# Kernel tuning notes

Measured on AMD Instinct MI355X. Metric: run time of the kernel, lower is better.

The kernel has to match this reference:

```python
import jax, jax.numpy as jnp
import numpy as np

N_NODES = 50000
N_EDGES = 800000
IN_DIM = 128
EMB = 64
EDGE_DIM = 6
N_LAYERS = 4
OUT_DIM = 1


def setup_inputs() -> dict:
    key = jax.random.key(0)
    ks = jax.random.split(key, 20)
    s = 0.05
    inp = {
        "x": jax.random.normal(ks[0], (N_NODES, IN_DIM), jnp.float32),
        "edge_index": jax.random.randint(ks[1], (2, N_EDGES), 0, N_NODES, jnp.int64),
        "edge_attr": jax.random.normal(ks[2], (N_EDGES, EDGE_DIM), jnp.float32),
        # input projection
        "lin_in_w": jax.random.normal(ks[3], (IN_DIM, EMB), jnp.float32) * s,
        "lin_in_b": jnp.zeros((EMB,), jnp.float32),
        # stacked per-layer MLP params: message MLP psi: (2*EMB+EDGE_DIM)->EMB->EMB
        "msg_w1": jax.random.normal(ks[4], (N_LAYERS, 2 * EMB + EDGE_DIM, EMB), jnp.float32) * s,
        "msg_b1": jnp.zeros((N_LAYERS, EMB), jnp.float32),
        "msg_w2": jax.random.normal(ks[5], (N_LAYERS, EMB, EMB), jnp.float32) * s,
        "msg_b2": jnp.zeros((N_LAYERS, EMB), jnp.float32),
        # update MLP phi: (2*EMB)->EMB->EMB
        "upd_w1": jax.random.normal(ks[6], (N_LAYERS, 2 * EMB, EMB), jnp.float32) * s,
        "upd_b1": jnp.zeros((N_LAYERS, EMB), jnp.float32),
        "upd_w2": jax.random.normal(ks[7], (N_LAYERS, EMB, EMB), jnp.float32) * s,
        "upd_b2": jnp.zeros((N_LAYERS, EMB), jnp.float32),
        # output head
        "pred_w": jax.random.normal(ks[8], (EMB, OUT_DIM), jnp.float32) * s,
        "pred_b": jnp.zeros((OUT_DIM,), jnp.float32),
    }
    return inp


def reference(x, edge_index, edge_attr, lin_in_w, lin_in_b,
              msg_w1, msg_b1, msg_w2, msg_b2,
              upd_w1, upd_b1, upd_w2, upd_b2,
              pred_w, pred_b):
    n = x.shape[0]
    src = edge_index[0]  # h_j: source nodes
    dst = edge_index[1]  # h_i: target nodes (aggregation index in PyG default flow)
    h = x @ lin_in_w + lin_in_b  # (n, EMB)
    n_layers = msg_w1.shape[0]
    for l in range(n_layers):
        # message: psi([h_i, h_j, e_ij])  -> (E, EMB)
        m = jnp.concatenate([h[dst], h[src], edge_attr], axis=-1)
        m = jax.nn.relu(m @ msg_w1[l] + msg_b1[l])
        m = jax.nn.relu(m @ msg_w2[l] + msg_b2[l])
        # aggregate: scatter-add over target nodes
        agg = jax.ops.segment_sum(m, dst, num_segments=n)
        # update: phi([h, m_i]) with residual connection (h = h + conv(h))
        u = jnp.concatenate([h, agg], axis=-1)
        u = jax.nn.relu(u @ upd_w1[l] + upd_b1[l])
        u = jax.nn.relu(u @ upd_w2[l] + upd_b2[l])
        h = h + u
    out = h @ pred_w + pred_b  # (n, OUT_DIM)
    return jnp.sum(out, axis=-2)  # (OUT_DIM,)
```

## Files before the change

kernel.cpp:

```cpp
#include <hip/hip_runtime.h>


typedef __attribute__((ext_vector_type(8))) short short8;
typedef __attribute__((ext_vector_type(4))) float float4v;

__device__ __forceinline__ unsigned short f2bf(float f) {
    unsigned int u = __float_as_uint(f);
    unsigned int r = u + 0x7fff + ((u >> 16) & 1);
    return (unsigned short)(r >> 16);
}
__device__ __forceinline__ float bf2f(unsigned short u) {
    return __uint_as_float(((unsigned int)u) << 16);
}

#define MFMA16(a, b, c) __builtin_amdgcn_mfma_f32_16x16x32_bf16(a, b, c, 0, 0, 0)

struct bfpair { short hi, lo; };
__device__ __forceinline__ bfpair wsplit(float wv) {
    bfpair p;
    unsigned short h = f2bf(wv);
    float hf = __uint_as_float(((unsigned int)h) << 16);
    p.hi = (short)h;
    p.lo = (short)f2bf(wv - hf);
    return p;
}

#define WP_TOTAL 106496
#define OFF_IN   0
#define OFF_PRE(l)  (8192  + (l) * 8192)
#define OFF_MW2(l)  (40960 + (l) * 4096)
#define OFF_UW1(l)  (57344 + (l) * 8192)
#define OFF_UW2(l)  (90112 + (l) * 4096)

__global__ __launch_bounds__(256) void k_wprep(const float* __restrict__ lin_w,
        const float* __restrict__ mw1, const float* __restrict__ mw2,
        const float* __restrict__ uw1, const float* __restrict__ uw2,
        unsigned short* __restrict__ H, unsigned short* __restrict__ L) {
    const int tid = blockIdx.x * 256 + threadIdx.x;
    if (tid >= WP_TOTAL) return;
    float val;
    if (tid < 8192) {
        int rem = tid;
        int nt = rem >> 11, kf = (rem >> 9) & 3;
        int lane = (rem >> 3) & 63, j = rem & 7;
        int k = kf * 32 + (lane >> 4) * 8 + j;
        val = lin_w[k * 64 + nt * 16 + (lane & 15)];
    } else if (tid < 40960) {
        int t = tid - 8192, layer = t >> 13, rem = t & 8191;
        int nt = rem >> 10, kf = (rem >> 9) & 1;
        int lane = (rem >> 3) & 63, j = rem & 7;
        int k = kf * 32 + (lane >> 4) * 8 + j;
        const float* w1 = mw1 + (size_t)layer * 134 * 64;
        val = (nt < 4) ? w1[k * 64 + nt * 16 + (lane & 15)]
                       : w1[(64 + k) * 64 + (nt - 4) * 16 + (lane & 15)];
    } else if (tid < 57344) {
        int t = tid - 40960, layer = t >> 12, rem = t & 4095;
        int nt = rem >> 10, kf = (rem >> 9) & 1;
        int lane = (rem >> 3) & 63, j = rem & 7;
        int k = kf * 32 + (lane >> 4) * 8 + j;
        val = mw2[(size_t)layer * 4096 + k * 64 + nt * 16 + (lane & 15)];
    } else if (tid < 90112) {
        int t = tid - 57344, layer = t >> 13, rem = t & 8191;
        int nt = rem >> 11, kf = (rem >> 9) & 3;
        int lane = (rem >> 3) & 63, j = rem & 7;
        int k = kf * 32 + (lane >> 4) * 8 + j;
        val = uw1[(size_t)layer * 8192 + k * 64 + nt * 16 + (lane & 15)];
    } else {
        int t = tid - 90112, layer = t >> 12, rem = t & 4095;
        int nt = rem >> 10, kf = (rem >> 9) & 1;
        int lane = (rem >> 3) & 63, j = rem & 7;
        int k = kf * 32 + (lane >> 4) * 8 + j;
        val = uw2[(size_t)layer * 4096 + k * 64 + nt * 16 + (lane & 15)];
    }
    bfpair p = wsplit(val);
    H[tid] = (unsigned short)p.hi;
    L[tid] = (unsigned short)p.lo;
}

#define LOADFRAG(dst, arr, nt, KF, kf) \
    dst = *(const short8*)&arr[((((nt) * (KF)) + (kf)) * 64 + lane) * 8]

__global__ __launch_bounds__(256) void k_hist(const int* __restrict__ dst,
        int* __restrict__ deg, int nEdges) {
    int e = blockIdx.x * blockDim.x + threadIdx.x;
    if (e < nEdges) atomicAdd(&deg[dst[e]], 1);
}

__global__ __launch_bounds__(256) void k_scan1(const int* __restrict__ deg,
        int* __restrict__ local, int* __restrict__ bsum, int nNodes) {
    __shared__ int sm[256];
    const int t = threadIdx.x;
    const int n = blockIdx.x * 256 + t;
    int v = (n < nNodes) ? deg[n] : 0;
    sm[t] = v;
    __syncthreads();
    for (int off = 1; off < 256; off <<= 1) {
        int u = (t >= off) ? sm[t - off] : 0;
        __syncthreads();
        sm[t] += u;
        __syncthreads();
    }
    if (n < nNodes) local[n] = sm[t] - v;
    if (t == 255) bsum[blockIdx.x] = sm[255];
}

__global__ __launch_bounds__(256) void k_scan2(int* __restrict__ bsum, int nB) {
    __shared__ int sm[256];
    const int t = threadIdx.x;
    int v = (t < nB) ? bsum[t] : 0;
    sm[t] = v;
    __syncthreads();
    for (int off = 1; off < 256; off <<= 1) {
        int u = (t >= off) ? sm[t - off] : 0;
        __syncthreads();
        sm[t] += u;
        __syncthreads();
    }
    if (t < nB) bsum[t] = sm[t] - v;
}

__global__ __launch_bounds__(256) void k_scan3(const int* __restrict__ local,
        const int* __restrict__ bsum, int* __restrict__ cursor, int nNodes) {
    int n = blockIdx.x * 256 + threadIdx.x;
    if (n < nNodes) cursor[n] = bsum[blockIdx.x] + local[n];
}

__global__ __launch_bounds__(256) void k_scatter(const int* __restrict__ src,
        const int* __restrict__ dst, const float* __restrict__ ea,
        int* __restrict__ cursor, int* __restrict__ col_src,
        int* __restrict__ dst_s, float* __restrict__ ea_s, int nEdges) {
    int e = blockIdx.x * blockDim.x + threadIdx.x;
    if (e < nEdges) {
        int d = dst[e];
        int pos = atomicAdd(&cursor[d], 1);
        col_src[pos] = src[e];
        dst_s[pos] = d;
        const float* p = ea + (size_t)e * 6;
        float* q = ea_s + (size_t)pos * 6;
#pragma unroll
        for (int j = 0; j < 6; ++j) q[j] = p[j];
    }
}


__global__ __launch_bounds__(256) void k_in(const float* __restrict__ x,
        const unsigned short* __restrict__ wh, const unsigned short* __restrict__ wl,
        const float* __restrict__ bia, float* __restrict__ h, int nNodes) {
    const int lane = threadIdx.x & 63;
    const int wib  = threadIdx.x >> 6;
    const int quad = lane >> 4, col = lane & 15;
    __shared__ unsigned short sm[4][16 * 136];
    unsigned short* __restrict__ mt = sm[wib];

    short8 bh[4][4], bl[4][4];
#pragma unroll
    for (int nt = 0; nt < 4; ++nt)
#pragma unroll
        for (int kf = 0; kf < 4; ++kf) {
            LOADFRAG(bh[nt][kf], wh, nt, 4, kf);
            LOADFRAG(bl[nt][kf], wl, nt, 4, kf);
        }
    float bv[4];
#pragma unroll
    for (int nt = 0; nt < 4; ++nt) bv[nt] = bia[nt * 16 + col];

    const int nTiles = (nNodes + 15) >> 4;
    const int wid = blockIdx.x * 4 + wib;
    const int nw  = gridDim.x * 4;
    for (int tile = wid; tile < nTiles; tile += nw) {
        const int base = tile * 16;
#pragma unroll
        for (int j = 0; j < 16; ++j) {
            int row = min(base + j, nNodes - 1);
            mt[j * 136 + lane]      = f2bf(x[(size_t)row * 128 + lane]);
            mt[j * 136 + 64 + lane] = f2bf(x[(size_t)row * 128 + 64 + lane]);
        }
        __builtin_amdgcn_s_waitcnt(0);
        short8 a[4];
#pragma unroll
        for (int kf = 0; kf < 4; ++kf)
            a[kf] = *(const short8*)&mt[col * 136 + kf * 32 + quad * 8];
#pragma unroll
        for (int nt = 0; nt < 4; ++nt) {
            float4v c = {0.f, 0.f, 0.f, 0.f};
#pragma unroll
            for (int kf = 0; kf < 4; ++kf) c = MFMA16(a[kf], bh[nt][kf], c);
#pragma unroll
            for (int kf = 0; kf < 4; ++kf) c = MFMA16(a[kf], bl[nt][kf], c);
#pragma unroll
            for (int r = 0; r < 4; ++r) {
                int row = base + quad * 4 + r;
                if (row < nNodes)
                    h[(size_t)row * 64 + nt * 16 + col] = c[r] + bv[nt];
            }
        }
    }
}

__global__ __launch_bounds__(256) void k_pre(const float* __restrict__ h,
        const unsigned short* __restrict__ wh, const unsigned short* __restrict__ wl,
        const float* __restrict__ b1m,
        unsigned short* __restrict__ P, unsigned short* __restrict__ Q,
        int nNodes) {
    const int lane = threadIdx.x & 63;
    const int wib  = threadIdx.x >> 6;
    const int quad = lane >> 4, col = lane & 15;
    __shared__ unsigned short sm[4][16 * 72];
    unsigned short* __restrict__ mt = sm[wib];

    short8 bh[8][2], bl[8][2];
#pragma unroll
    for (int nt = 0; nt < 8; ++nt)
#pragma unroll
        for (int kf = 0; kf < 2; ++kf) {
            LOADFRAG(bh[nt][kf], wh, nt, 2, kf);
            LOADFRAG(bl[nt][kf], wl, nt, 2, kf);
        }
    float bv1[4];
#pragma unroll
    for (int nt = 0; nt < 4; ++nt) bv1[nt] = b1m[nt * 16 + col];

    const int nTiles = (nNodes + 15) >> 4;
    const int wid = blockIdx.x * 4 + wib;
    const int nw  = gridDim.x * 4;
    for (int tile = wid; tile < nTiles; tile += nw) {
        const int base = tile * 16;
#pragma unroll
        for (int j = 0; j < 16; ++j) {
            int row = min(base + j, nNodes - 1);
            mt[j * 72 + lane] = f2bf(h[(size_t)row * 64 + lane]);
        }
        __builtin_amdgcn_s_waitcnt(0);
        short8 a0 = *(const short8*)&mt[col * 72 + quad * 8];
        short8 a1 = *(const short8*)&mt[col * 72 + 32 + quad * 8];
#pragma unroll
        for (int nt = 0; nt < 8; ++nt) {
            float4v c = {0.f, 0.f, 0.f, 0.f};
            c = MFMA16(a0, bh[nt][0], c);
            c = MFMA16(a1, bh[nt][1], c);
            c = MFMA16(a0, bl[nt][0], c);
            c = MFMA16(a1, bl[nt][1], c);
            unsigned short* __restrict__ outp = (nt < 4) ? P : Q;
            const int nc = (nt & 3) * 16 + col;
            const float badd = (nt < 4) ? bv1[nt & 3] : 0.f;
#pragma unroll
            for (int r = 0; r < 4; ++r) {
                int row = base + quad * 4 + r;
                if (row < nNodes) outp[(size_t)row * 64 + nc] = f2bf(c[r] + badd);
            }
        }
    }
}

__global__ __launch_bounds__(256) void k_upd1(const float* __restrict__ h,
        const float* __restrict__ agg,
        const unsigned short* __restrict__ wh, const unsigned short* __restrict__ wl,
        const float* __restrict__ b1, float* __restrict__ tv, int nNodes) {
    const int lane = threadIdx.x & 63;
    const int wib  = threadIdx.x >> 6;
    const int quad = lane >> 4, col = lane & 15;
    __shared__ unsigned short sm[4][16 * 136];
    unsigned short* __restrict__ mt = sm[wib];

    short8 bh[4][4], bl[4][4];
#pragma unroll
    for (int nt = 0; nt < 4; ++nt)
#pragma unroll
        for (int kf = 0; kf < 4; ++kf) {
            LOADFRAG(bh[nt][kf], wh, nt, 4, kf);
            LOADFRAG(bl[nt][kf], wl, nt, 4, kf);
        }
    float bv[4];
#pragma unroll
    for (int nt = 0; nt < 4; ++nt) bv[nt] = b1[nt * 16 + col];

    const int nTiles = (nNodes + 15) >> 4;
    const int wid = blockIdx.x * 4 + wib;
    const int nw  = gridDim.x * 4;
    for (int tile = wid; tile < nTiles; tile += nw) {
        const int base = tile * 16;
#pragma unroll
        for (int j = 0; j < 16; ++j) {
            int row = min(base + j, nNodes - 1);
            mt[j * 136 + lane]      = f2bf(h[(size_t)row * 64 + lane]);
            mt[j * 136 + 64 + lane] = f2bf(agg[(size_t)row * 64 + lane]);
        }
        __builtin_amdgcn_s_waitcnt(0);
        short8 a[4];
#pragma unroll
        for (int kf = 0; kf < 4; ++kf)
            a[kf] = *(const short8*)&mt[col * 136 + kf * 32 + quad * 8];
#pragma unroll
        for (int nt = 0; nt < 4; ++nt) {
            float4v c = {0.f, 0.f, 0.f, 0.f};
#pragma unroll
            for (int kf = 0; kf < 4; ++kf) c = MFMA16(a[kf], bh[nt][kf], c);
#pragma unroll
            for (int kf = 0; kf < 4; ++kf) c = MFMA16(a[kf], bl[nt][kf], c);
#pragma unroll
            for (int r = 0; r < 4; ++r) {
                int row = base + quad * 4 + r;
                if (row < nNodes)
                    tv[(size_t)row * 64 + nt * 16 + col] = fmaxf(c[r] + bv[nt], 0.f);
            }
        }
    }
}

__global__ __launch_bounds__(256) void k_upd2(float* __restrict__ h,
        float* __restrict__ tv,
        const unsigned short* __restrict__ wh, const unsigned short* __restrict__ wl,
        const float* __restrict__ b2, float* __restrict__ colsum,
        int nNodes, int doCS) {
    const int lane = threadIdx.x & 63;
    const int wib  = threadIdx.x >> 6;
    const int quad = lane >> 4, col = lane & 15;
    __shared__ unsigned short sm[4][16 * 72];
    unsigned short* __restrict__ mt = sm[wib];

    short8 bh[4][2], bl[4][2];
#pragma unroll
    for (int nt = 0; nt < 4; ++nt)
#pragma unroll
        for (int kf = 0; kf < 2; ++kf) {
            LOADFRAG(bh[nt][kf], wh, nt, 2, kf);
            LOADFRAG(bl[nt][kf], wl, nt, 2, kf);
        }
    float bv[4];
#pragma unroll
    for (int nt = 0; nt < 4; ++nt) bv[nt] = b2[nt * 16 + col];

    float cs0 = 0.f, cs1 = 0.f, cs2 = 0.f, cs3 = 0.f;
    const int nTiles = (nNodes + 15) >> 4;
    const int wid = blockIdx.x * 4 + wib;
    const int nw  = gridDim.x * 4;
    for (int tile = wid; tile < nTiles; tile += nw) {
        const int base = tile * 16;
#pragma unroll
        for (int j = 0; j < 16; ++j) {
            int row = min(base + j, nNodes - 1);
            mt[j * 72 + lane] = f2bf(tv[(size_t)row * 64 + lane]);
        }
        __builtin_amdgcn_s_waitcnt(0);
#pragma unroll
        for (int j = 0; j < 16; ++j) {
            int row = base + j;
            if (row < nNodes) tv[(size_t)row * 64 + lane] = 0.f;
        }
        short8 a0 = *(const short8*)&mt[col * 72 + quad * 8];
        short8 a1 = *(const short8*)&mt[col * 72 + 32 + quad * 8];
#pragma unroll
        for (int nt = 0; nt < 4; ++nt) {
            float4v c = {0.f, 0.f, 0.f, 0.f};
            c = MFMA16(a0, bh[nt][0], c);
            c = MFMA16(a1, bh[nt][1], c);
            c = MFMA16(a0, bl[nt][0], c);
            c = MFMA16(a1, bl[nt][1], c);
#pragma unroll
            for (int r = 0; r < 4; ++r) {
                int row = base + quad * 4 + r;
                if (row < nNodes) {
                    float* hp = &h[(size_t)row * 64 + nt * 16 + col];
                    float hn = *hp + fmaxf(c[r] + bv[nt], 0.f);
                    *hp = hn;
                    cs0 += (nt == 0) ? hn : 0.f;
                    cs1 += (nt == 1) ? hn : 0.f;
                    cs2 += (nt == 2) ? hn : 0.f;
                    cs3 += (nt == 3) ? hn : 0.f;
                }
            }
        }
    }
    if (doCS) {
        cs0 += __shfl_xor(cs0, 16); cs0 += __shfl_xor(cs0, 32);
        cs1 += __shfl_xor(cs1, 16); cs1 += __shfl_xor(cs1, 32);
        cs2 += __shfl_xor(cs2, 16); cs2 += __shfl_xor(cs2, 32);
        cs3 += __shfl_xor(cs3, 16); cs3 += __shfl_xor(cs3, 32);
        const float tot = (quad == 0) ? cs0 : (quad == 1) ? cs1
                        : (quad == 2) ? cs2 : cs3;
        atomicAdd(&colsum[lane], tot);
    }
}

#define EST 72

__global__ __launch_bounds__(256, 4) void k_edge(const unsigned short* __restrict__ P,
        const unsigned short* __restrict__ Q, const float* __restrict__ ea_s,
        const int* __restrict__ col_src, const int* __restrict__ dst_s,
        const float* __restrict__ w1e,
        const unsigned short* __restrict__ wh, const unsigned short* __restrict__ wl,
        const float* __restrict__ b2,
        float* __restrict__ agg, int nEdges) {
    const int lane = threadIdx.x & 63;
    const int wib  = threadIdx.x >> 6;
    const int wid  = blockIdx.x * 4 + wib;
    const int nw   = gridDim.x * 4;
    const int quad = lane >> 4;
    const int col  = lane & 15;
    const int li   = lane & 31;

    __shared__ unsigned short m1b[4][32 * EST];
    __shared__ unsigned short wB[8192];
    unsigned short* __restrict__ mt = m1b[wib];

    {
        const short8* __restrict__ sH = (const short8*)wh;
        const short8* __restrict__ sL = (const short8*)wl;
        short8* __restrict__ dB = (short8*)wB;
        for (int i = threadIdx.x; i < 512; i += 256) {
            dB[i]       = sH[i];
            dB[512 + i] = sL[i];
        }
    }
    __syncthreads();

    float w1ec[6];
#pragma unroll
    for (int j = 0; j < 6; ++j) w1ec[j] = w1e[j * 64 + lane];

    float b2v[4];
#pragma unroll
    for (int nt = 0; nt < 4; ++nt) b2v[nt] = b2[nt * 16 + col];

    const int nBatch = (nEdges + 31) >> 5;
    const int per = nBatch / nw, rem = nBatch % nw;
    const int btLo = wid * per + min(wid, rem);
    const int btHi = btLo + per + (wid < rem ? 1 : 0);

    for (int bt = btLo; bt < btHi; ++bt) {
        const int base = __builtin_amdgcn_readfirstlane(bt << 5);
        const int gidx = min(base + li, nEdges - 1);
        const int vdj = dst_s[gidx];
        const int vsj = col_src[gidx];
        const int vprev = __shfl_up(vdj, 1);
        unsigned long long bmask =
            __ballot(lane < 32 && (li == 0 || vdj != vprev));
        bmask |= (1ull << 32) | 1ull;

#pragma unroll
        for (int j = 0; j < 32; ++j) {
            const int d = __builtin_amdgcn_readlane(vdj, j);
            const int s = __builtin_amdgcn_readlane(vsj, j);
            const int idx = min(base + j, nEdges - 1);
            float t = bf2f(P[(size_t)d * 64 + lane]) +
                      bf2f(Q[(size_t)s * 64 + lane]);
            const float* eap = ea_s + (size_t)idx * 6;
#pragma unroll
            for (int jj = 0; jj < 6; ++jj) t = fmaf(eap[jj], w1ec[jj], t);
            mt[j * EST + lane] = f2bf(fmaxf(t, 0.f));
        }
        __builtin_amdgcn_s_waitcnt(0);

        short8 a00 = *(const short8*)&mt[col * EST + quad * 8];
        short8 a01 = *(const short8*)&mt[col * EST + 32 + quad * 8];
        short8 a10 = *(const short8*)&mt[(16 + col) * EST + quad * 8];
        short8 a11 = *(const short8*)&mt[(16 + col) * EST + 32 + quad * 8];

        float4v m2v[2][4];
#pragma unroll
        for (int nt = 0; nt < 4; ++nt) {
            const short8 h0 = *(const short8*)&wB[((nt * 2 + 0) * 64 + lane) * 8];
            const short8 h1 = *(const short8*)&wB[((nt * 2 + 1) * 64 + lane) * 8];
            const short8 l0 = *(const short8*)&wB[4096 + ((nt * 2 + 0) * 64 + lane) * 8];
            const short8 l1 = *(const short8*)&wB[4096 + ((nt * 2 + 1) * 64 + lane) * 8];
            float4v c0 = {0.f, 0.f, 0.f, 0.f};
            float4v c1 = {0.f, 0.f, 0.f, 0.f};
            c0 = MFMA16(a00, h0, c0);
            c0 = MFMA16(a01, h1, c0);
            c0 = MFMA16(a00, l0, c0);
            c0 = MFMA16(a01, l1, c0);
            c1 = MFMA16(a10, h0, c1);
            c1 = MFMA16(a11, h1, c1);
            c1 = MFMA16(a10, l0, c1);
            c1 = MFMA16(a11, l1, c1);
#pragma unroll
            for (int r = 0; r < 4; ++r) {
                const bool v0 = base + (quad * 4 + r) < nEdges;
                const bool v1 = base + 16 + (quad * 4 + r) < nEdges;
                m2v[0][nt][r] = v0 ? fmaxf(c0[r] + b2v[nt], 0.f) : 0.f;
                m2v[1][nt][r] = v1 ? fmaxf(c1[r] + b2v[nt], 0.f) : 0.f;
            }
        }

        int r0 = 0;
        while (r0 < 32) {
            const int nid = __builtin_amdgcn_readlane(vdj, r0);
            const int r1 = r0 + 1 + (int)__builtin_ctzll(bmask >> (r0 + 1));
            float s0 = 0.f, s1 = 0.f, s2 = 0.f, s3 = 0.f;
#pragma unroll
            for (int t = 0; t < 2; ++t)
#pragma unroll
                for (int r = 0; r < 4; ++r) {
                    const int R = t * 16 + quad * 4 + r;
                    const bool in = (R >= r0) && (R < r1);
                    s0 += in ? m2v[t][0][r] : 0.f;
                    s1 += in ? m2v[t][1][r] : 0.f;
                    s2 += in ? m2v[t][2][r] : 0.f;
                    s3 += in ? m2v[t][3][r] : 0.f;
                }
            s0 += __shfl_xor(s0, 16); s0 += __shfl_xor(s0, 32);
            s1 += __shfl_xor(s1, 16); s1 += __shfl_xor(s1, 32);
            s2 += __shfl_xor(s2, 16); s2 += __shfl_xor(s2, 32);
            s3 += __shfl_xor(s3, 16); s3 += __shfl_xor(s3, 32);
            const float tot = (quad == 0) ? s0 : (quad == 1) ? s1
                            : (quad == 2) ? s2 : s3;
            atomicAdd(&agg[(size_t)nid * 64 + lane], tot);
            r0 = r1;
        }
    }
}

__global__ void k_out(const float* __restrict__ colsum, const float* __restrict__ pw,
                      const float* __restrict__ pb, float* __restrict__ out, int nNodes) {
    const int lane = threadIdx.x;
    float v = colsum[lane] * pw[lane];
#pragma unroll
    for (int off = 32; off; off >>= 1) v += __shfl_down(v, off);
    if (lane == 0) out[0] = v + (float)nNodes * pb[0];
}

extern "C" void kernel_launch(void* const* d_in, const int* in_sizes, int n_in,
                              void* d_out, int out_size, void* d_ws, size_t ws_size,
                              hipStream_t stream) {
    const float* x     = (const float*)d_in[0];
    const int*   ei    = (const int*)d_in[1];
    const float* ea    = (const float*)d_in[2];
    const float* lin_w = (const float*)d_in[3];
    const float* lin_b = (const float*)d_in[4];
    const float* mw1   = (const float*)d_in[5];
    const float* mb1   = (const float*)d_in[6];
    const float* mw2   = (const float*)d_in[7];
    const float* mb2   = (const float*)d_in[8];
    const float* uw1   = (const float*)d_in[9];
    const float* ub1   = (const float*)d_in[10];
    const float* uw2   = (const float*)d_in[11];
    const float* ub2   = (const float*)d_in[12];
    const float* pw    = (const float*)d_in[13];
    const float* pb    = (const float*)d_in[14];

    const int nNodes = in_sizes[0] / 128;
    const int nEdges = in_sizes[1] / 2;
    const int* src = ei;
    const int* dst = ei + nEdges;

    float* h       = (float*)d_ws;
    float* agg     = h   + (size_t)nNodes * 64;
    float* ea_s    = agg + (size_t)nNodes * 64;
    float* colsum  = ea_s + (size_t)nEdges * 6;
    unsigned short* Pb  = (unsigned short*)(colsum + 64);
    unsigned short* Qb  = Pb + (size_t)nNodes * 64;
    unsigned short* wpH = Qb + (size_t)nNodes * 64;
    unsigned short* wpL = wpH + WP_TOTAL;
    int*   deg     = (int*)(wpL + WP_TOTAL);
    int*   cursor  = deg + nNodes;
    int*   local   = cursor + nNodes;
    int*   bsum    = local + nNodes;
    int*   col_src = bsum + 256;
    int*   dst_s   = col_src + nEdges;

    const int NB_T    = 392;
    const int NB_EDGE = 2048;
    const int NB_FLAT = (nEdges + 255) / 256;
    const int NB_SCAN = (nNodes + 255) / 256;

    hipMemsetAsync(deg, 0, (size_t)nNodes * sizeof(int), stream);
    hipMemsetAsync(colsum, 0, 64 * sizeof(float), stream);
    hipMemsetAsync(agg, 0, (size_t)nNodes * 64 * sizeof(float), stream);
    k_hist<<<NB_FLAT, 256, 0, stream>>>(dst, deg, nEdges);
    k_scan1<<<NB_SCAN, 256, 0, stream>>>(deg, local, bsum, nNodes);
    k_scan2<<<1, 256, 0, stream>>>(bsum, NB_SCAN);
    k_scan3<<<NB_SCAN, 256, 0, stream>>>(local, bsum, cursor, nNodes);
    k_scatter<<<NB_FLAT, 256, 0, stream>>>(src, dst, ea, cursor, col_src, dst_s, ea_s, nEdges);
    k_wprep<<<(WP_TOTAL + 255) / 256, 256, 0, stream>>>(lin_w, mw1, mw2, uw1, uw2, wpH, wpL);

    k_in<<<NB_T, 256, 0, stream>>>(x, wpH + OFF_IN, wpL + OFF_IN, lin_b, h, nNodes);

    for (int l = 0; l < 4; ++l) {
        k_pre<<<NB_T, 256, 0, stream>>>(h, wpH + OFF_PRE(l), wpL + OFF_PRE(l),
            mb1 + l * 64, Pb, Qb, nNodes);
        k_edge<<<NB_EDGE, 256, 0, stream>>>(Pb, Qb, ea_s, col_src, dst_s,
            mw1 + (size_t)l * 134 * 64 + 128 * 64,
            wpH + OFF_MW2(l), wpL + OFF_MW2(l), mb2 + l * 64, agg, nEdges);
        k_upd1<<<NB_T, 256, 0, stream>>>(h, agg,
            wpH + OFF_UW1(l), wpL + OFF_UW1(l), ub1 + l * 64, agg, nNodes);
        k_upd2<<<NB_T, 256, 0, stream>>>(h, agg,
            wpH + OFF_UW2(l), wpL + OFF_UW2(l), ub2 + l * 64,
            colsum, nNodes, (l == 3) ? 1 : 0);
    }

    k_out<<<1, 64, 0, stream>>>(colsum, pw, pb, (float*)d_out, nNodes);
}
```

Baseline: 642.0 us.

## Stage weight fragments in LDS, split edge scatter into pos+gather, raise node grid

Node kernels (k_in, k_pre, k_upd1, k_upd2) now copy split-bf16 weight fragments into shared memory once per block and read them from LDS at each MFMA. They no longer hold those fragments in registers, which cuts VGPR pressure so more waves can be resident. The edge CSR build is split into a kernel that records the inverse permutation and a gather kernel that writes sorted arrays with coalesced stores, replacing scattered multi-word writes. The node-kernel grid grows from 392 to 768 blocks. In exchange this adds an extra kernel launch, up to 32KB of LDS per block, and an LDS read per MFMA operand.

```diff
diff --git a/kernel.cpp b/kernel.cpp
--- a/kernel.cpp
+++ b/kernel.cpp
@@ -77,8 +77,20 @@
     L[tid] = (unsigned short)p.lo;
 }
 
-#define LOADFRAG(dst, arr, nt, KF, kf) \
-    dst = *(const short8*)&arr[((((nt) * (KF)) + (kf)) * 64 + lane) * 8]
+#define STAGE_WB(NFRAG) \
+    { const short8* __restrict__ sH = (const short8*)wh; \
+      const short8* __restrict__ sL = (const short8*)wl; \
+      short8* __restrict__ dB = (short8*)wB; \
+      for (int i = threadIdx.x; i < (NFRAG) * 64; i += 256) { \
+          dB[i] = sH[i]; \
+          dB[(NFRAG) * 64 + i] = sL[i]; \
+      } } \
+    __syncthreads();
+
+#define WB_HI(nt, KF, kf) \
+    (*(const short8*)&wB[(((nt) * (KF) + (kf)) * 64 + lane) * 8])
+#define WB_LO(NFRAG, nt, KF, kf) \
+    (*(const short8*)&wB[((NFRAG) + (nt) * (KF) + (kf)) * 512 + lane * 8])
 
 __global__ __launch_bounds__(256) void k_hist(const int* __restrict__ dst,
         int* __restrict__ deg, int nEdges) {
@@ -125,20 +137,29 @@
     if (n < nNodes) cursor[n] = bsum[blockIdx.x] + local[n];
 }
 
-__global__ __launch_bounds__(256) void k_scatter(const int* __restrict__ src,
-        const int* __restrict__ dst, const float* __restrict__ ea,
-        int* __restrict__ cursor, int* __restrict__ col_src,
-        int* __restrict__ dst_s, float* __restrict__ ea_s, int nEdges) {
+__global__ __launch_bounds__(256) void k_pos(const int* __restrict__ dst,
+        int* __restrict__ cursor, int* __restrict__ inv, int nEdges) {
     int e = blockIdx.x * blockDim.x + threadIdx.x;
     if (e < nEdges) {
-        int d = dst[e];
-        int pos = atomicAdd(&cursor[d], 1);
-        col_src[pos] = src[e];
-        dst_s[pos] = d;
-        const float* p = ea + (size_t)e * 6;
-        float* q = ea_s + (size_t)pos * 6;
-#pragma unroll
-        for (int j = 0; j < 6; ++j) q[j] = p[j];
+        int pos = atomicAdd(&cursor[dst[e]], 1);
+        inv[pos] = e;
+    }
+}
+
+__global__ __launch_bounds__(256) void k_gather(const int* __restrict__ inv,
+        const int* __restrict__ src, const int* __restrict__ dst,
+        const float* __restrict__ ea,
+        int* __restrict__ col_src, int* __restrict__ dst_s,
+        float* __restrict__ ea_s, int nEdges) {
+    int p = blockIdx.x * blockDim.x + threadIdx.x;
+    if (p < nEdges) {
+        int e = inv[p];
+        col_src[p] = src[e];
+        dst_s[p]   = dst[e];
+        const float* q = ea + (size_t)e * 6;
+        float* o = ea_s + (size_t)p * 6;
+#pragma unroll
+        for (int j = 0; j < 6; ++j) o[j] = q[j];
     }
 }
 
@@ -150,16 +171,11 @@
     const int wib  = threadIdx.x >> 6;
     const int quad = lane >> 4, col = lane & 15;
     __shared__ unsigned short sm[4][16 * 136];
+    __shared__ unsigned short wB[16384];
     unsigned short* __restrict__ mt = sm[wib];
 
-    short8 bh[4][4], bl[4][4];
-#pragma unroll
-    for (int nt = 0; nt < 4; ++nt)
-#pragma unroll
-        for (int kf = 0; kf < 4; ++kf) {
-            LOADFRAG(bh[nt][kf], wh, nt, 4, kf);
-            LOADFRAG(bl[nt][kf], wl, nt, 4, kf);
-        }
+    STAGE_WB(16)
+
     float bv[4];
 #pragma unroll
     for (int nt = 0; nt < 4; ++nt) bv[nt] = bia[nt * 16 + col];
@@ -184,9 +200,9 @@
         for (int nt = 0; nt < 4; ++nt) {
             float4v c = {0.f, 0.f, 0.f, 0.f};
 #pragma unroll
-            for (int kf = 0; kf < 4; ++kf) c = MFMA16(a[kf], bh[nt][kf], c);
-#pragma unroll
-            for (int kf = 0; kf < 4; ++kf) c = MFMA16(a[kf], bl[nt][kf], c);
+            for (int kf = 0; kf < 4; ++kf) c = MFMA16(a[kf], WB_HI(nt, 4, kf), c);
+#pragma unroll
+            for (int kf = 0; kf < 4; ++kf) c = MFMA16(a[kf], WB_LO(16, nt, 4, kf), c);
 #pragma unroll
             for (int r = 0; r < 4; ++r) {
                 int row = base + quad * 4 + r;
@@ -206,16 +222,11 @@
     const int wib  = threadIdx.x >> 6;
     const int quad = lane >> 4, col = lane & 15;
     __shared__ unsigned short sm[4][16 * 72];
+    __shared__ unsigned short wB[16384];
     unsigned short* __restrict__ mt = sm[wib];
 
-    short8 bh[8][2], bl[8][2];
-#pragma unroll
-    for (int nt = 0; nt < 8; ++nt)
-#pragma unroll
-        for (int kf = 0; kf < 2; ++kf) {
-            LOADFRAG(bh[nt][kf], wh, nt, 2, kf);
-            LOADFRAG(bl[nt][kf], wl, nt, 2, kf);
-        }
+    STAGE_WB(16)
+
     float bv1[4];
 #pragma unroll
     for (int nt = 0; nt < 4; ++nt) bv1[nt] = b1m[nt * 16 + col];
@@ -236,10 +247,10 @@
 #pragma unroll
         for (int nt = 0; nt < 8; ++nt) {
             float4v c = {0.f, 0.f, 0.f, 0.f};
-            c = MFMA16(a0, bh[nt][0], c);
-            c = MFMA16(a1, bh[nt][1], c);
-            c = MFMA16(a0, bl[nt][0], c);
-            c = MFMA16(a1, bl[nt][1], c);
+            c = MFMA16(a0, WB_HI(nt, 2, 0), c);
+            c = MFMA16(a1, WB_HI(nt, 2, 1), c);
+            c = MFMA16(a0, WB_LO(16, nt, 2, 0), c);
+            c = MFMA16(a1, WB_LO(16, nt, 2, 1), c);
             unsigned short* __restrict__ outp = (nt < 4) ? P : Q;
             const int nc = (nt & 3) * 16 + col;
             const float badd = (nt < 4) ? bv1[nt & 3] : 0.f;
@@ -260,16 +271,11 @@
     const int wib  = threadIdx.x >> 6;
     const int quad = lane >> 4, col = lane & 15;
     __shared__ unsigned short sm[4][16 * 136];
+    __shared__ unsigned short wB[16384];
     unsigned short* __restrict__ mt = sm[wib];
 
-    short8 bh[4][4], bl[4][4];
-#pragma unroll
-    for (int nt = 0; nt < 4; ++nt)
-#pragma unroll
-        for (int kf = 0; kf < 4; ++kf) {
-            LOADFRAG(bh[nt][kf], wh, nt, 4, kf);
-            LOADFRAG(bl[nt][kf], wl, nt, 4, kf);
-        }
+    STAGE_WB(16)
+
     float bv[4];
 #pragma unroll
     for (int nt = 0; nt < 4; ++nt) bv[nt] = b1[nt * 16 + col];
@@ -294,9 +300,9 @@
         for (int nt = 0; nt < 4; ++nt) {
             float4v c = {0.f, 0.f, 0.f, 0.f};
 #pragma unroll
-            for (int kf = 0; kf < 4; ++kf) c = MFMA16(a[kf], bh[nt][kf], c);
-#pragma unroll
-            for (int kf = 0; kf < 4; ++kf) c = MFMA16(a[kf], bl[nt][kf], c);
+            for (int kf = 0; kf < 4; ++kf) c = MFMA16(a[kf], WB_HI(nt, 4, kf), c);
+#pragma unroll
+            for (int kf = 0; kf < 4; ++kf) c = MFMA16(a[kf], WB_LO(16, nt, 4, kf), c);
 #pragma unroll
             for (int r = 0; r < 4; ++r) {
                 int row = base + quad * 4 + r;
@@ -316,16 +322,11 @@
     const int wib  = threadIdx.x >> 6;
     const int quad = lane >> 4, col = lane & 15;
     __shared__ unsigned short sm[4][16 * 72];
+    __shared__ unsigned short wB[8192];
     unsigned short* __restrict__ mt = sm[wib];
 
-    short8 bh[4][2], bl[4][2];
-#pragma unroll
-    for (int nt = 0; nt < 4; ++nt)
-#pragma unroll
-        for (int kf = 0; kf < 2; ++kf) {
-            LOADFRAG(bh[nt][kf], wh, nt, 2, kf);
-            LOADFRAG(bl[nt][kf], wl, nt, 2, kf);
-        }
+    STAGE_WB(8)
+
     float bv[4];
 #pragma unroll
     for (int nt = 0; nt < 4; ++nt) bv[nt] = b2[nt * 16 + col];
@@ -352,10 +353,10 @@
 #pragma unroll
         for (int nt = 0; nt < 4; ++nt) {
             float4v c = {0.f, 0.f, 0.f, 0.f};
-            c = MFMA16(a0, bh[nt][0], c);
-            c = MFMA16(a1, bh[nt][1], c);
-            c = MFMA16(a0, bl[nt][0], c);
-            c = MFMA16(a1, bl[nt][1], c);
+            c = MFMA16(a0, WB_HI(nt, 2, 0), c);
+            c = MFMA16(a1, WB_HI(nt, 2, 1), c);
+            c = MFMA16(a0, WB_LO(8, nt, 2, 0), c);
+            c = MFMA16(a1, WB_LO(8, nt, 2, 1), c);
 #pragma unroll
             for (int r = 0; r < 4; ++r) {
                 int row = base + quad * 4 + r;
@@ -557,8 +558,9 @@
     int*   bsum    = local + nNodes;
     int*   col_src = bsum + 256;
     int*   dst_s   = col_src + nEdges;
-
-    const int NB_T    = 392;
+    int*   inv     = dst_s + nEdges;
+
+    const int NB_T    = 768;
     const int NB_EDGE = 2048;
     const int NB_FLAT = (nEdges + 255) / 256;
     const int NB_SCAN = (nNodes + 255) / 256;
@@ -570,7 +572,8 @@
     k_scan1<<<NB_SCAN, 256, 0, stream>>>(deg, local, bsum, nNodes);
     k_scan2<<<1, 256, 0, stream>>>(bsum, NB_SCAN);
     k_scan3<<<NB_SCAN, 256, 0, stream>>>(local, bsum, cursor, nNodes);
-    k_scatter<<<NB_FLAT, 256, 0, stream>>>(src, dst, ea, cursor, col_src, dst_s, ea_s, nEdges);
+    k_pos<<<NB_FLAT, 256, 0, stream>>>(dst, cursor, inv, nEdges);
+    k_gather<<<NB_FLAT, 256, 0, stream>>>(inv, src, dst, ea, col_src, dst_s, ea_s, nEdges);
     k_wprep<<<(WP_TOTAL + 255) / 256, 256, 0, stream>>>(lin_w, mw1, mw2, uw1, uw2, wpH, wpL);
 
     k_in<<<NB_T, 256, 0, stream>>>(x, wpH + OFF_IN, wpL + OFF_IN, lin_b, h, nNodes);
```

After: 706.6 us. +10.1%, slower.
